# Kernel tuning notes

Measured on AMD Instinct MI355X. Metric: run time of the kernel, lower is better.

Reference implementation:

```python
import jax, jax.numpy as jnp
import numpy as np

DIM = 6
S = 2 ** DIM  # 64 nonzero B-spline basis products per edge (degree-1 spline)


def _bits():
    # [S, DIM] binary offsets enumerating the 2^dim corners of the spline cell
    return jnp.asarray(((np.arange(S)[:, None] >> np.arange(DIM)[None, :]) & 1).astype(np.int32))


def spline_basis(u, ks):
    # u: [E, DIM] pseudo-coords in [0,1); open B-spline, degree 1
    bits = _bits()                      # [S, DIM]
    v = u * (ks - 1)                    # [E, DIM]
    lo = jnp.floor(v)
    frac = v - lo                       # fractional position in cell
    lo = lo.astype(jnp.int32)
    # basis[e,s] = prod_d (frac if bit else 1-frac)
    basis = jnp.prod(jnp.where(bits[None].astype(bool), frac[:, None, :], 1.0 - frac[:, None, :]), axis=-1)  # [E,S]
    pos = jnp.clip(lo[:, None, :] + bits[None, :, :], 0, ks - 1)  # [E,S,DIM]
    strides = (ks ** jnp.arange(DIM)).astype(jnp.int32)           # per-dim stride in flattened kernel
    idx = jnp.sum(pos * strides[None, None, :], axis=-1)          # [E,S] in [0, ks^DIM)
    return basis, idx


def spline_conv(x, src, dst, basis, idx, W, Wr, b, n):
    # x:[N,in], W:[K,in,out], basis/idx:[E,S]. Mean aggregation + root weight + bias (PyG defaults).
    x_src = x[src]                                  # [E,in] gather
    out_ch = W.shape[2]
    acc0 = jnp.zeros((x_src.shape[0], out_ch), x.dtype)

    def body(acc, bs_is):
        bs, ii = bs_is                              # [E], [E]
        m = jnp.einsum('ei,eio->eo', x_src, W[ii])  # basis-indexed weight gather + per-edge matvec
        return acc + bs[:, None] * m, None

    msg, _ = jax.lax.scan(body, acc0, (basis.T, idx.T))   # loop over S=64 spline corners
    agg = jax.ops.segment_sum(msg, dst, num_segments=n)   # scatter-add to target nodes
    deg = jax.ops.segment_sum(jnp.ones(dst.shape, x.dtype), dst, num_segments=n)
    agg = agg / jnp.clip(deg, 1.0)[:, None]                # aggr='mean'
    return agg + x @ Wr + b


def setup_inputs() -> dict:
    key = jax.random.key(0)
    ks = jax.random.split(key, 16)
    N, E = 4096, 16384
    x = jax.random.normal(ks[0], (N, 32), jnp.float32)
    edge_index = jax.random.randint(ks[1], (2, E), 0, N, jnp.int32)
    edge_attr = jax.random.uniform(ks[2], (E, DIM), jnp.float32)

    def wk(k, K, cin, cout):
        return jax.random.normal(k, (K, cin, cout), jnp.float32) * (1.0 / np.sqrt(cin * S))

    def wr(k, cin, cout):
        return jax.random.normal(k, (cin, cout), jnp.float32) * (1.0 / np.sqrt(cin))

    return {
        'x': x, 'edge_index': edge_index, 'edge_attr': edge_attr,
        'W1': wk(ks[3], 3 ** DIM, 32, 128), 'Wr1': wr(ks[4], 32, 128), 'b1': jnp.zeros((128,), jnp.float32),
        'W3': wk(ks[5], 3 ** DIM, 128, 128), 'Wr3': wr(ks[6], 128, 128), 'b3': jnp.zeros((128,), jnp.float32),
        'W6': wk(ks[7], 5 ** DIM, 128, 64), 'Wr6': wr(ks[8], 128, 64), 'b6': jnp.zeros((64,), jnp.float32),
        'W7': wk(ks[9], 7 ** DIM, 64, 13), 'Wr7': wr(ks[10], 64, 13), 'b7': jnp.zeros((13,), jnp.float32),
    }


def reference(x, edge_index, edge_attr, W1, Wr1, b1, W3, Wr3, b3, W6, Wr6, b6, W7, Wr7, b7):
    src, dst = edge_index[0], edge_index[1]
    n = x.shape[0]
    basis3, idx3 = spline_basis(edge_attr, 3)  # shared by conv1 and conv3 (same kernel_size)
    h = spline_conv(x, src, dst, basis3, idx3, W1, Wr1, b1, n)
    h = spline_conv(h, src, dst, basis3, idx3, W3, Wr3, b3, n)
    basis5, idx5 = spline_basis(edge_attr, 5)
    h = spline_conv(h, src, dst, basis5, idx5, W6, Wr6, b6, n)
    basis7, idx7 = spline_basis(edge_attr, 7)
    h = spline_conv(h, src, dst, basis7, idx7, W7, Wr7, b7, n)
    h = jax.nn.elu(h)
    return jax.nn.log_softmax(h, axis=1)
```

## Files before the change

kernel.cpp:

```cpp
#include <hip/hip_runtime.h>
#include <hip/hip_bf16.h>
#include <cstdint>
#include <cstddef>

constexpr int SDIM = 6;
constexpr int SCOR = 64;
constexpr int REP3 = 8;
constexpr int CAP3 = 4096;
constexpr int CAP5 = 512;
constexpr int CAP7 = 128;
typedef unsigned short u16;
typedef unsigned char u8;
typedef __attribute__((ext_vector_type(8))) short bf16x8;
typedef __attribute__((ext_vector_type(4))) float f32x4;
typedef __attribute__((ext_vector_type(2))) float f32x2;
typedef __attribute__((ext_vector_type(4))) int i32x4;

__device__ __forceinline__ float bf2f(u16 h) {
    union { unsigned u; float f; } v; v.u = ((unsigned)h) << 16; return v.f;
}
__device__ __forceinline__ u16 f2bf(float f) {
    union { float f; unsigned u; } v; v.f = f;
    unsigned r = v.u + 0x7fffu + ((v.u >> 16) & 1u);
    return (u16)(r >> 16);
}

__device__ __forceinline__ u8 f2e4m3(float f) {
#if __has_builtin(__builtin_amdgcn_cvt_pk_fp8_f32)
    return (u8)(__builtin_amdgcn_cvt_pk_fp8_f32(f, 0.0f, 0, false) & 0xff);
#else
    unsigned u = __float_as_uint(f);
    unsigned s = (u >> 24) & 0x80;
    int exp = (int)((u >> 23) & 0xff) - 127;
    unsigned man = u & 0x7fffff;
    if (exp > 8 || (exp == 8 && man >= 0x700000)) return (u8)(s | 0x7e);
    if (exp >= -6) {
        unsigned m = man >> 20;
        unsigned rest = man & 0xfffff;
        if (rest > 0x80000 || (rest == 0x80000 && (m & 1))) m++;
        unsigned v = (((unsigned)(exp + 7)) << 3) + m;
        if (v > 0x7e) v = 0x7e;
        return (u8)(s | v);
    }
    if (exp < -10) return (u8)s;
    float af = __uint_as_float(u & 0x7fffffff);
    int M = (int)(af * 512.0f + 0.5f);
    if (M > 7) M = 7;
    return (u8)(s | M);
#endif
}

__device__ __forceinline__ void e4m3x4_acc(unsigned w, float* a) {
#if __has_builtin(__builtin_amdgcn_cvt_pk_f32_fp8)
    f32x2 lo = __builtin_amdgcn_cvt_pk_f32_fp8((int)w, false);
    f32x2 hi = __builtin_amdgcn_cvt_pk_f32_fp8((int)w, true);
    a[0] += lo.x; a[1] += lo.y; a[2] += hi.x; a[3] += hi.y;
#else
    #pragma unroll
    for (int j = 0; j < 4; j++) {
        unsigned b = (w >> (8 * j)) & 0xff;
        unsigned s = (b & 0x80) << 24;
        unsigned em = b & 0x7f;
        float v = (em >= 8)
            ? __uint_as_float((((em >> 3) + 120) << 23) | ((em & 7) << 20))
            : (float)em * (1.0f / 512.0f);
        a[j] += __uint_as_float(__float_as_uint(v) | s);
    }
#endif
}

template <int KS>
__device__ __forceinline__ void keybasis(const float* u, int s, int& key, float& basis) {
    int idx = 0, str = 1;
    float b = 1.0f;
    #pragma unroll
    for (int d = 0; d < SDIM; d++) {
        float v = u[d] * (KS - 1);
        float fl = floorf(v);
        float fr = v - fl;
        int bit = (s >> d) & 1;
        int pos = (int)fl + bit;
        pos = min(max(pos, 0), KS - 1);
        idx += pos * str;
        str *= KS;
        b *= bit ? fr : (1.0f - fr);
    }
    key = idx;
    basis = b;
}

__global__ __launch_bounds__(256) void prep_kernel(int* __restrict__ zb, int nz,
                                                   const float* __restrict__ xin,
                                                   u16* __restrict__ xbf, int n4) {
    int i = blockIdx.x * blockDim.x + threadIdx.x;
    if (i < nz) zb[i] = 0;
    if (i < n4) {
        float4 v = ((const float4*)xin)[i];
        ushort4 o;
        o.x = f2bf(v.x); o.y = f2bf(v.y); o.z = f2bf(v.z); o.w = f2bf(v.w);
        ((ushort4*)xbf)[i] = o;
    }
}

__global__ __launch_bounds__(256) void deg_kernel(const int* __restrict__ dst,
                                                  int* __restrict__ degi, int E) {
    int e = blockIdx.x * blockDim.x + threadIdx.x;
    if (e < E) atomicAdd(&degi[dst[e]], 1);
}

__global__ __launch_bounds__(1024) void scan_kernel(int* __restrict__ counts,
                                                    int* __restrict__ offs, int K) {
    __shared__ int sums[1024];
    int t = threadIdx.x;
    int chunk = (K + 1023) / 1024;
    int a0 = t * chunk;
    int a1 = min(a0 + chunk, K);
    int s = 0;
    for (int j = a0; j < a1; j++) s += counts[j];
    sums[t] = s;
    __syncthreads();
    for (int off = 1; off < 1024; off <<= 1) {
        int v = (t >= off) ? sums[t - off] : 0;
        __syncthreads();
        sums[t] += v;
        __syncthreads();
    }
    int run = (t == 0) ? 0 : sums[t - 1];
    for (int j = a0; j < a1; j++) {
        int c = counts[j];
        offs[j] = run;
        counts[j] = run;
        run += c;
    }
    if (t == 1023) offs[K] = run;
}

__global__ __launch_bounds__(256) void fill_all(const float* __restrict__ ea,
                                                const int* __restrict__ src,
                                                const int* __restrict__ dst,
                                                int* __restrict__ ecur,
                                                int* __restrict__ cnt3r, int2* __restrict__ pP3,
                                                int* __restrict__ cnt5, int2* __restrict__ pP5,
                                                int* __restrict__ cnt7, int2* __restrict__ pP7,
                                                int P) {
    int gid = blockIdx.x * blockDim.x + threadIdx.x;
    if (gid >= P) return;
    int e = gid >> 6;
    int lane = threadIdx.x & 63;
    int rep = blockIdx.x & (REP3 - 1);
    float u[SDIM];
    #pragma unroll
    for (int d = 0; d < SDIM; d++) u[d] = ea[e * SDIM + d];
    int node = src[e];
    int er = 0;
    if (lane == 0) er = atomicAdd(&ecur[dst[e]], 1);
    er = __shfl(er, 0);
    int packed = (node << 20) | (er * SCOR + lane);
    int k; float b; int slot;
    keybasis<3>(u, lane, k, b);
    slot = (k * REP3 + rep) * CAP3 + atomicAdd(&cnt3r[k * REP3 + rep], 1);
    pP3[slot] = make_int2(packed, __float_as_int(b));
    keybasis<5>(u, lane, k, b);
    slot = k * CAP5 + atomicAdd(&cnt5[k], 1);
    pP5[slot] = make_int2(packed, __float_as_int(b));
    keybasis<7>(u, lane, k, b);
    slot = k * CAP7 + atomicAdd(&cnt7[k], 1);
    pP7[slot] = make_int2(packed, __float_as_int(b));
}

template <int IN, int OUT, int WAVES, int WN, int CAP>
__global__ __launch_bounds__(WAVES * 64) void conv_mfma_r(
    const u16* __restrict__ xbf, const float* __restrict__ W,
    const int* __restrict__ cnt, const int2* __restrict__ pairP,
    u8* __restrict__ mpart) {
    constexpr int NT = WAVES * 64;
    constexpr int WM = WAVES / WN;
    constexpr int OUT16 = (OUT + 15) & ~15;
    static_assert(OUT == OUT16, "conv_mfma_r requires OUT multiple of 16");
    constexpr int WSTR = OUT + 2;
    constexpr int NF = OUT16 / 16;
    constexpr int NFW = NF / WN;
    constexpr int KS = IN / 32;
    constexpr int TW = NFW * 16;
    constexpr int TSTR = TW + 16;
    constexpr int CHW = TW / 16;
    static_assert(TSTR % 16 == 0, "row stride must be 16B aligned");
    static_assert((IN * OUT) % NT == 0, "staging divisibility");

    __shared__ u16 Wlds[IN * WSTR];
    __shared__ u8 tall[WAVES][16 * TSTR];

    int k = blockIdx.x;
    int idx = k * gridDim.y + blockIdx.y;
    int p0 = idx * CAP;
    int p1 = p0 + cnt[idx];
    if (p0 >= p1) return;

    int t = threadIdx.x;
    int wid = t >> 6, lane = t & 63;
    int wm = wid % WM, wn = wid / WM;
    int l15 = lane & 15, l4 = lane >> 4;
    u8* twave = tall[wid];

    const float* Wg = W + (size_t)k * IN * OUT;
    #pragma unroll
    for (int f0 = 0; f0 < IN * OUT; f0 += NT) {
        int f = f0 + t;
        int i = f / OUT, o = f % OUT;
        Wlds[i * WSTR + o] = f2bf(Wg[f]);
    }
    __syncthreads();

    bf16x8 breg[KS][NFW];
    #pragma unroll
    for (int ks = 0; ks < KS; ks++) {
        #pragma unroll
        for (int nf = 0; nf < NFW; nf++) {
            int col = (wn * NFW + nf) * 16 + l15;
            int rbase = ks * 32 + l4 * 8;
            bf16x8 b;
            #pragma unroll
            for (int j = 0; j < 8; j++)
                ((u16*)&b)[j] = Wlds[(rbase + j) * WSTR + col];
            breg[ks][nf] = b;
        }
    }

    constexpr int STRIDE = WM * 16;
    int t0 = p0 + wm * 16;
    if (t0 >= p1) return;

    int2 meta = pairP[min(t0 + l15, p1 - 1)];
    bf16x8 a[KS];
    {
        const u16* xrow = xbf + (size_t)((unsigned)meta.x >> 20) * IN + l4 * 8;
        #pragma unroll
        for (int ks = 0; ks < KS; ks++) a[ks] = *(const bf16x8*)(xrow + ks * 32);
    }

    while (true) {
        int np = min(16, p1 - t0);
        float basv = (l15 < np) ? __int_as_float(meta.y) * 64.0f : 0.0f;
        int srv = meta.x & 0xFFFFF;
        int tn = t0 + STRIDE;
        bool has = tn < p1;
        int2 metaN = meta;
        if (has) metaN = pairP[min(tn + l15, p1 - 1)];

        f32x4 acc[NFW];
        #pragma unroll
        for (int nf = 0; nf < NFW; nf++)
            acc[nf] = f32x4{0.f, 0.f, 0.f, 0.f};
        #pragma unroll
        for (int ks = 0; ks < KS; ks++) {
            #pragma unroll
            for (int nf = 0; nf < NFW; nf++)
                acc[nf] = __builtin_amdgcn_mfma_f32_16x16x32_bf16(a[ks], breg[ks][nf], acc[nf], 0, 0, 0);
        }

        bf16x8 aN[KS];
        if (has) {
            const u16* xrowN = xbf + (size_t)((unsigned)metaN.x >> 20) * IN + l4 * 8;
            #pragma unroll
            for (int ks = 0; ks < KS; ks++) aN[ks] = *(const bf16x8*)(xrowN + ks * 32);
        }

        #pragma unroll
        for (int nf = 0; nf < NFW; nf++) {
            #pragma unroll
            for (int r = 0; r < 4; r++) {
                int pl = l4 * 4 + r;
                float bs = __shfl(basv, pl);
                twave[pl * TSTR + nf * 16 + l15] = f2e4m3(acc[nf][r] * bs);
            }
        }

        #pragma unroll
        for (int it = 0; it < (16 * CHW + 63) / 64; it++) {
            int cid = it * 64 + lane;
            int row = cid / CHW, ch = cid % CHW;
            int srr = __shfl(srv, row);
            if (cid < 16 * CHW && row < np)
                __builtin_nontemporal_store(
                    *(const i32x4*)&twave[row * TSTR + ch * 16],
                    (i32x4*)(mpart + (size_t)srr * OUT16 + wn * TW + ch * 16));
        }

        if (!has) break;
        t0 = tn;
        meta = metaN;
        #pragma unroll
        for (int ks = 0; ks < KS; ks++) a[ks] = aN[ks];
    }
}

__global__ __launch_bounds__(256) void conv_mfma_w7(
    const u16* __restrict__ xbf, const float* __restrict__ W,
    const int* __restrict__ cnt, const int2* __restrict__ pairP,
    u16* __restrict__ mpart, int K) {
    constexpr int IN = 64, OUT = 13, OUT16 = 16;
    __shared__ u16 WT[4][16 * 72];
    __shared__ u16 tbAll[4][16 * 24];
    int t = threadIdx.x, wid = t >> 6, lane = t & 63;
    int k = blockIdx.x * 4 + wid;
    if (k >= K) return;
    int p0 = k * CAP7, p1 = p0 + cnt[k];
    if (p0 >= p1) return;
    u16* tb = tbAll[wid];
    u16* wt = WT[wid];

    int l15 = lane & 15, l4 = lane >> 4;
    const float* Wg = W + (size_t)k * (IN * OUT);
    for (int f = lane; f < IN * OUT; f += 64) {
        int r = f / OUT, c = f - r * OUT;
        wt[c * 72 + r] = f2bf(Wg[f]);
    }
    bf16x8 breg[2];
    #pragma unroll
    for (int ks = 0; ks < 2; ks++)
        breg[ks] = (l15 < OUT) ? *(const bf16x8*)&wt[l15 * 72 + ks * 32 + l4 * 8]
                               : bf16x8{0, 0, 0, 0, 0, 0, 0, 0};

    for (int t0 = p0; t0 < p1; t0 += 16) {
        int np = min(16, p1 - t0);
        int2 meta = pairP[min(t0 + l15, p1 - 1)];
        float basv = (l15 < np) ? __int_as_float(meta.y) : 0.0f;
        int srv = meta.x & 0xFFFFF;
        const u16* xrow = xbf + (size_t)((unsigned)meta.x >> 20) * IN + l4 * 8;
        f32x4 acc = f32x4{0.f, 0.f, 0.f, 0.f};
        #pragma unroll
        for (int ks = 0; ks < 2; ks++) {
            bf16x8 a = *(const bf16x8*)(xrow + ks * 32);
            acc = __builtin_amdgcn_mfma_f32_16x16x32_bf16(a, breg[ks], acc, 0, 0, 0);
        }
        #pragma unroll
        for (int r = 0; r < 4; r++) {
            int pl = l4 * 4 + r;
            float bs = __shfl(basv, pl);
            tb[pl * 24 + l15] = f2bf(acc[r] * bs);
        }
        {
            int row = lane >> 1, ch = lane & 1;
            int srr = __shfl(srv, row);
            if (lane < np * 2)
                __builtin_nontemporal_store(
                    *(const bf16x8*)&tb[row * 24 + ch * 8],
                    (bf16x8*)(mpart + (size_t)srr * OUT16 + ch * 8));
        }
    }
}

template <int IN, int OUT, int OUT16, bool HEAD, bool FP8>
__global__ __launch_bounds__(256) void reduce_wave(
    const void* __restrict__ mpartv, const int* __restrict__ eoff,
    const float* __restrict__ xin, const float* __restrict__ Wr,
    const float* __restrict__ bias, float* __restrict__ hout,
    u16* __restrict__ hbf, int N) {
    constexpr int CH = OUT16 / 16;
    constexpr int RG = 64 / CH;
    __shared__ float sm[4][OUT16];

    int t = threadIdx.x, wid = t >> 6, lane = t & 63;
    int nodeLocal = wid >> 1, hf = wid & 1;
    int n = blockIdx.x * 2 + nodeLocal;

    int e0 = 0, e1 = 0;
    if (n < N) { e0 = eoff[n]; e1 = eoff[n + 1]; }
    int R = (e1 - e0) * SCOR;
    size_t rs = (size_t)e0 * SCOR;
    int rg = lane / CH, ch = lane % CH;

    float a[16];
    #pragma unroll
    for (int j = 0; j < 16; j++) a[j] = 0.0f;
    #pragma unroll 4
    for (int r = rg + hf * RG; r < R; r += RG * 2) {
        if constexpr (FP8) {
            const u8* mp = (const u8*)mpartv + (rs + r) * OUT16 + ch * 16;
            i32x4 w = __builtin_nontemporal_load((const i32x4*)mp);
            e4m3x4_acc((unsigned)w.x, a + 0);
            e4m3x4_acc((unsigned)w.y, a + 4);
            e4m3x4_acc((unsigned)w.z, a + 8);
            e4m3x4_acc((unsigned)w.w, a + 12);
        } else {
            const u16* mp = (const u16*)mpartv + (rs + r) * OUT16 + ch * 16;
            bf16x8 v0 = __builtin_nontemporal_load((const bf16x8*)mp);
            bf16x8 v1 = __builtin_nontemporal_load((const bf16x8*)(mp + 8));
            #pragma unroll
            for (int j = 0; j < 8; j++) a[j] += bf2f(((const u16*)&v0)[j]);
            #pragma unroll
            for (int j = 0; j < 8; j++) a[8 + j] += bf2f(((const u16*)&v1)[j]);
        }
    }
    #pragma unroll
    for (int m = CH; m < 64; m <<= 1) {
        #pragma unroll
        for (int j = 0; j < 16; j++) a[j] += __shfl_xor(a[j], m);
    }
    if (lane < CH) {
        #pragma unroll
        for (int j = 0; j < 16; j++) sm[wid][lane * 16 + j] = a[j];
    }
    __syncthreads();

    if (n >= N) return;
    int dg = e1 - e0;
    float dinv = 1.0f / (float)(dg < 1 ? 1 : dg);
    if constexpr (FP8) dinv *= (1.0f / 64.0f);
    const float* xr = xin + (size_t)n * IN;

    if constexpr (!HEAD) {
        int o = hf * (OUT / 2) + lane;
        if (lane < OUT / 2) {
            float s = (sm[nodeLocal * 2][o] + sm[nodeLocal * 2 + 1][o]) * dinv + bias[o];
            #pragma unroll 8
            for (int i = 0; i < IN; i++) s += xr[i] * Wr[i * OUT + o];
            hout[(size_t)n * OUT + o] = s;
            if (hbf) hbf[(size_t)n * OUT + o] = f2bf(s);
        }
    } else {
        if (hf == 0 && lane < 16) {
            float s = 0.0f;
            if (lane < OUT) {
                s = (sm[nodeLocal * 2][lane] + sm[nodeLocal * 2 + 1][lane]) * dinv + bias[lane];
                #pragma unroll 8
                for (int i = 0; i < IN; i++) s += xr[i] * Wr[i * OUT + lane];
            }
            sm[wid][lane] = s;
            float v[13];
            float mx = -1e30f;
            #pragma unroll
            for (int c = 0; c < 13; c++) {
                float z = sm[wid][c];
                z = z > 0.0f ? z : (expf(z) - 1.0f);
                v[c] = z;
                mx = fmaxf(mx, z);
            }
            float sum = 0.0f;
            #pragma unroll
            for (int c = 0; c < 13; c++) sum += expf(v[c] - mx);
            float lse = mx + logf(sum);
            if (lane < 13) hout[(size_t)n * 13 + lane] = v[lane] - lse;
        }
    }
}

extern "C" void kernel_launch(void* const* d_in, const int* in_sizes, int n_in,
                              void* d_out, int out_size, void* d_ws, size_t ws_size,
                              hipStream_t stream) {
    const float* x   = (const float*)d_in[0];
    const int*   ei  = (const int*)d_in[1];
    const float* ea  = (const float*)d_in[2];
    const float* W1  = (const float*)d_in[3];
    const float* Wr1 = (const float*)d_in[4];
    const float* b1  = (const float*)d_in[5];
    const float* W3  = (const float*)d_in[6];
    const float* Wr3 = (const float*)d_in[7];
    const float* b3  = (const float*)d_in[8];
    const float* W6  = (const float*)d_in[9];
    const float* Wr6 = (const float*)d_in[10];
    const float* b6  = (const float*)d_in[11];
    const float* W7  = (const float*)d_in[12];
    const float* Wr7 = (const float*)d_in[13];
    const float* b7  = (const float*)d_in[14];

    const int N = in_sizes[0] / 32;
    const int E = in_sizes[1] / 2;
    const int* src = ei;
    const int* dst = ei + E;
    (void)n_in; (void)out_size; (void)ws_size;

    const int K3 = 729, K5 = 15625, K7 = 117649;
    const int P = E * SCOR;

    const int NC3 = K3 * REP3;
    const int totalZ = N + NC3 + K5 + K7;

    char* ws = (char*)d_ws;
    size_t off = 0;
    auto alloc = [&](size_t bytes) {
        void* p = ws + off;
        off += (bytes + 255) & ~(size_t)255;
        return p;
    };
    int*   zb    = (int*)alloc((size_t)totalZ * 4);
    int*   degi  = zb;
    int*   cnt3r = zb + N;
    int*   cnt5  = cnt3r + NC3;
    int*   cnt7  = cnt5 + K5;
    int*   eoff  = (int*)alloc((size_t)(N + 1) * 4);
    int2*  pP3   = (int2*)alloc((size_t)NC3 * CAP3 * 8);
    int2*  pP5   = (int2*)alloc((size_t)K5 * CAP5 * 8);
    int2*  pP7   = (int2*)alloc((size_t)K7 * CAP7 * 8);
    float* h1    = (float*)alloc((size_t)N * 128 * 4);
    float* h3    = (float*)alloc((size_t)N * 128 * 4);
    float* h6    = (float*)alloc((size_t)N * 64 * 4);
    u16*   xbf1  = (u16*)alloc((size_t)N * 32 * 2);
    u16*   hbf1  = (u16*)alloc((size_t)N * 128 * 2);
    u16*   hbf3  = (u16*)alloc((size_t)N * 128 * 2);
    u16*   hbf6  = (u16*)alloc((size_t)N * 64 * 2);
    u8*    mpart = (u8*)alloc((size_t)P * 128);

    dim3 blk(256);
    dim3 egrid((E + 255) / 256);
    dim3 pgrid((P + 255) / 256);
    int rgrid = (N + 1) / 2;

    int n4 = N * 32 / 4;
    prep_kernel<<<(max(totalZ, n4) + 255) / 256, blk, 0, stream>>>(zb, totalZ, x, xbf1, n4);

    deg_kernel<<<egrid, blk, 0, stream>>>(dst, degi, E);
    scan_kernel<<<1, 1024, 0, stream>>>(degi, eoff, N);

    fill_all<<<pgrid, blk, 0, stream>>>(ea, src, dst, degi, cnt3r, pP3, cnt5, pP5, cnt7, pP7, P);

    conv_mfma_r<32, 128, 8, 2, CAP3><<<dim3(K3, REP3), dim3(512), 0, stream>>>(
        xbf1, W1, cnt3r, pP3, mpart);
    reduce_wave<32, 128, 128, false, true><<<rgrid, blk, 0, stream>>>(mpart, eoff, x, Wr1, b1, h1, hbf1, N);

    conv_mfma_r<128, 128, 8, 2, CAP3><<<dim3(K3, REP3), dim3(512), 0, stream>>>(
        hbf1, W3, cnt3r, pP3, mpart);
    reduce_wave<128, 128, 128, false, true><<<rgrid, blk, 0, stream>>>(mpart, eoff, h1, Wr3, b3, h3, hbf3, N);

    conv_mfma_r<128, 64, 4, 2, CAP5><<<dim3(K5, 1), blk, 0, stream>>>(
        hbf3, W6, cnt5, pP5, mpart);
    reduce_wave<128, 64, 64, false, true><<<rgrid, blk, 0, stream>>>(mpart, eoff, h3, Wr6, b6, h6, hbf6, N);

    conv_mfma_w7<<<(K7 + 3) / 4, blk, 0, stream>>>(hbf6, W7, cnt7, pP7, (u16*)mpart, K7);
    reduce_wave<64, 13, 16, true, false><<<rgrid, blk, 0, stream>>>(mpart, eoff, h6, Wr7, b7, (float*)d_out, nullptr, N);
}
```

Measured before the change: 945.0 us.

## Replace CSR edge offsets with fixed-capacity per-node slots and bf16 root inputs

Drops the degree-count and single-block scan kernels. Each node now gets a fixed CAPN=32 slot region in the partial-message buffer, and the edge rank comes straight from the atomic in fill_all. The pair metadata is repacked so the basis is stored as bf16 next to a 16-bit source node, and the root-weight path reads bf16 activations instead of keeping separate fp32 copies. This removes two serial launches and some fp32 traffic, but it assumes in-degree ≤32 and node ids below 65536, enlarges mpart, and lowers basis and root-input precision.

Result: no change. 933.2 us (-1.3%).

```diff
diff --git a/kernel.cpp b/kernel.cpp
--- a/kernel.cpp
+++ b/kernel.cpp
@@ -9,6 +9,7 @@
 constexpr int CAP3 = 4096;
 constexpr int CAP5 = 512;
 constexpr int CAP7 = 128;
+constexpr int CAPN = 32;
 typedef unsigned short u16;
 typedef unsigned char u8;
 typedef __attribute__((ext_vector_type(8))) short bf16x8;
@@ -102,43 +103,10 @@
     }
 }
 
-__global__ __launch_bounds__(256) void deg_kernel(const int* __restrict__ dst,
-                                                  int* __restrict__ degi, int E) {
-    int e = blockIdx.x * blockDim.x + threadIdx.x;
-    if (e < E) atomicAdd(&degi[dst[e]], 1);
-}
-
-__global__ __launch_bounds__(1024) void scan_kernel(int* __restrict__ counts,
-                                                    int* __restrict__ offs, int K) {
-    __shared__ int sums[1024];
-    int t = threadIdx.x;
-    int chunk = (K + 1023) / 1024;
-    int a0 = t * chunk;
-    int a1 = min(a0 + chunk, K);
-    int s = 0;
-    for (int j = a0; j < a1; j++) s += counts[j];
-    sums[t] = s;
-    __syncthreads();
-    for (int off = 1; off < 1024; off <<= 1) {
-        int v = (t >= off) ? sums[t - off] : 0;
-        __syncthreads();
-        sums[t] += v;
-        __syncthreads();
-    }
-    int run = (t == 0) ? 0 : sums[t - 1];
-    for (int j = a0; j < a1; j++) {
-        int c = counts[j];
-        offs[j] = run;
-        counts[j] = run;
-        run += c;
-    }
-    if (t == 1023) offs[K] = run;
-}
-
 __global__ __launch_bounds__(256) void fill_all(const float* __restrict__ ea,
                                                 const int* __restrict__ src,
                                                 const int* __restrict__ dst,
-                                                int* __restrict__ ecur,
+                                                int* __restrict__ degi,
                                                 int* __restrict__ cnt3r, int2* __restrict__ pP3,
                                                 int* __restrict__ cnt5, int2* __restrict__ pP5,
                                                 int* __restrict__ cnt7, int2* __restrict__ pP7,
@@ -152,20 +120,26 @@
     #pragma unroll
     for (int d = 0; d < SDIM; d++) u[d] = ea[e * SDIM + d];
     int node = src[e];
+    int dn = dst[e];
     int er = 0;
-    if (lane == 0) er = atomicAdd(&ecur[dst[e]], 1);
+    if (lane == 0) er = atomicAdd(&degi[dn], 1);
     er = __shfl(er, 0);
-    int packed = (node << 20) | (er * SCOR + lane);
+    int er64 = (dn * CAPN + er) * SCOR + lane;
     int k; float b; int slot;
     keybasis<3>(u, lane, k, b);
+    int2 m;
+    m.x = er64;
+    m.y = ((int)f2bf(b) << 16) | node;
     slot = (k * REP3 + rep) * CAP3 + atomicAdd(&cnt3r[k * REP3 + rep], 1);
-    pP3[slot] = make_int2(packed, __float_as_int(b));
+    pP3[slot] = m;
     keybasis<5>(u, lane, k, b);
+    m.y = ((int)f2bf(b) << 16) | node;
     slot = k * CAP5 + atomicAdd(&cnt5[k], 1);
-    pP5[slot] = make_int2(packed, __float_as_int(b));
+    pP5[slot] = m;
     keybasis<7>(u, lane, k, b);
+    m.y = ((int)f2bf(b) << 16) | node;
     slot = k * CAP7 + atomicAdd(&cnt7[k], 1);
-    pP7[slot] = make_int2(packed, __float_as_int(b));
+    pP7[slot] = m;
 }
 
 template <int IN, int OUT, int WAVES, int WN, int CAP>
@@ -233,15 +207,15 @@
     int2 meta = pairP[min(t0 + l15, p1 - 1)];
     bf16x8 a[KS];
     {
-        const u16* xrow = xbf + (size_t)((unsigned)meta.x >> 20) * IN + l4 * 8;
+        const u16* xrow = xbf + (size_t)((unsigned)meta.y & 0xFFFF) * IN + l4 * 8;
         #pragma unroll
         for (int ks = 0; ks < KS; ks++) a[ks] = *(const bf16x8*)(xrow + ks * 32);
     }
 
     while (true) {
         int np = min(16, p1 - t0);
-        float basv = (l15 < np) ? __int_as_float(meta.y) * 64.0f : 0.0f;
-        int srv = meta.x & 0xFFFFF;
+        float basv = (l15 < np) ? bf2f((u16)((unsigned)meta.y >> 16)) * 64.0f : 0.0f;
+        int srv = meta.x;
         int tn = t0 + STRIDE;
         bool has = tn < p1;
         int2 metaN = meta;
@@ -260,7 +234,7 @@
 
         bf16x8 aN[KS];
         if (has) {
-            const u16* xrowN = xbf + (size_t)((unsigned)metaN.x >> 20) * IN + l4 * 8;
+            const u16* xrowN = xbf + (size_t)((unsigned)metaN.y & 0xFFFF) * IN + l4 * 8;
             #pragma unroll
             for (int ks = 0; ks < KS; ks++) aN[ks] = *(const bf16x8*)(xrowN + ks * 32);
         }
@@ -324,9 +298,9 @@
     for (int t0 = p0; t0 < p1; t0 += 16) {
         int np = min(16, p1 - t0);
         int2 meta = pairP[min(t0 + l15, p1 - 1)];
-        float basv = (l15 < np) ? __int_as_float(meta.y) : 0.0f;
-        int srv = meta.x & 0xFFFFF;
-        const u16* xrow = xbf + (size_t)((unsigned)meta.x >> 20) * IN + l4 * 8;
+        float basv = (l15 < np) ? bf2f((u16)((unsigned)meta.y >> 16)) : 0.0f;
+        int srv = meta.x;
+        const u16* xrow = xbf + (size_t)((unsigned)meta.y & 0xFFFF) * IN + l4 * 8;
         f32x4 acc = f32x4{0.f, 0.f, 0.f, 0.f};
         #pragma unroll
         for (int ks = 0; ks < 2; ks++) {
@@ -352,9 +326,9 @@
 
 template <int IN, int OUT, int OUT16, bool HEAD, bool FP8>
 __global__ __launch_bounds__(256) void reduce_wave(
-    const void* __restrict__ mpartv, const int* __restrict__ eoff,
-    const float* __restrict__ xin, const float* __restrict__ Wr,
-    const float* __restrict__ bias, float* __restrict__ hout,
+    const void* __restrict__ mpartv, const int* __restrict__ degi,
+    const u16* __restrict__ xinbf, const float* __restrict__ Wr,
+    const float* __restrict__ bias, float* __restrict__ outf,
     u16* __restrict__ hbf, int N) {
     constexpr int CH = OUT16 / 16;
     constexpr int RG = 64 / CH;
@@ -364,10 +338,9 @@
     int nodeLocal = wid >> 1, hf = wid & 1;
     int n = blockIdx.x * 2 + nodeLocal;
 
-    int e0 = 0, e1 = 0;
-    if (n < N) { e0 = eoff[n]; e1 = eoff[n + 1]; }
-    int R = (e1 - e0) * SCOR;
-    size_t rs = (size_t)e0 * SCOR;
+    int dg = (n < N) ? degi[n] : 0;
+    int R = dg * SCOR;
+    size_t rs = (size_t)n * CAPN * SCOR;
     int rg = lane / CH, ch = lane % CH;
 
     float a[16];
@@ -404,19 +377,17 @@
     __syncthreads();
 
     if (n >= N) return;
-    int dg = e1 - e0;
     float dinv = 1.0f / (float)(dg < 1 ? 1 : dg);
     if constexpr (FP8) dinv *= (1.0f / 64.0f);
-    const float* xr = xin + (size_t)n * IN;
+    const u16* xr = xinbf + (size_t)n * IN;
 
     if constexpr (!HEAD) {
         int o = hf * (OUT / 2) + lane;
         if (lane < OUT / 2) {
             float s = (sm[nodeLocal * 2][o] + sm[nodeLocal * 2 + 1][o]) * dinv + bias[o];
             #pragma unroll 8
-            for (int i = 0; i < IN; i++) s += xr[i] * Wr[i * OUT + o];
-            hout[(size_t)n * OUT + o] = s;
-            if (hbf) hbf[(size_t)n * OUT + o] = f2bf(s);
+            for (int i = 0; i < IN; i++) s += bf2f(xr[i]) * Wr[i * OUT + o];
+            hbf[(size_t)n * OUT + o] = f2bf(s);
         }
     } else {
         if (hf == 0 && lane < 16) {
@@ -424,7 +395,7 @@
             if (lane < OUT) {
                 s = (sm[nodeLocal * 2][lane] + sm[nodeLocal * 2 + 1][lane]) * dinv + bias[lane];
                 #pragma unroll 8
-                for (int i = 0; i < IN; i++) s += xr[i] * Wr[i * OUT + lane];
+                for (int i = 0; i < IN; i++) s += bf2f(xr[i]) * Wr[i * OUT + lane];
             }
             sm[wid][lane] = s;
             float v[13];
@@ -440,7 +411,7 @@
             #pragma unroll
             for (int c = 0; c < 13; c++) sum += expf(v[c] - mx);
             float lse = mx + logf(sum);
-            if (lane < 13) hout[(size_t)n * 13 + lane] = v[lane] - lse;
+            if (lane < 13) outf[(size_t)n * 13 + lane] = v[lane] - lse;
         }
     }
 }
@@ -488,44 +459,40 @@
     int*   cnt3r = zb + N;
     int*   cnt5  = cnt3r + NC3;
     int*   cnt7  = cnt5 + K5;
-    int*   eoff  = (int*)alloc((size_t)(N + 1) * 4);
     int2*  pP3   = (int2*)alloc((size_t)NC3 * CAP3 * 8);
     int2*  pP5   = (int2*)alloc((size_t)K5 * CAP5 * 8);
     int2*  pP7   = (int2*)alloc((size_t)K7 * CAP7 * 8);
-    float* h1    = (float*)alloc((size_t)N * 128 * 4);
-    float* h3    = (float*)alloc((size_t)N * 128 * 4);
-    float* h6    = (float*)alloc((size_t)N * 64 * 4);
     u16*   xbf1  = (u16*)alloc((size_t)N * 32 * 2);
     u16*   hbf1  = (u16*)alloc((size_t)N * 128 * 2);
     u16*   hbf3  = (u16*)alloc((size_t)N * 128 * 2);
     u16*   hbf6  = (u16*)alloc((size_t)N * 64 * 2);
-    u8*    mpart = (u8*)alloc((size_t)P * 128);
+    u8*    mpart = (u8*)alloc((size_t)N * CAPN * SCOR * 128);
 
     dim3 blk(256);
-    dim3 egrid((E + 255) / 256);
     dim3 pgrid((P + 255) / 256);
     int rgrid = (N + 1) / 2;
 
     int n4 = N * 32 / 4;
     prep_kernel<<<(max(totalZ, n4) + 255) / 256, blk, 0, stream>>>(zb, totalZ, x, xbf1, n4);
 
-    deg_kernel<<<egrid, blk, 0, stream>>>(dst, degi, E);
-    scan_kernel<<<1, 1024, 0, stream>>>(degi, eoff, N);
-
     fill_all<<<pgrid, blk, 0, stream>>>(ea, src, dst, degi, cnt3r, pP3, cnt5, pP5, cnt7, pP7, P);
 
     conv_mfma_r<32, 128, 8, 2, CAP3><<<dim3(K3, REP3), dim3(512), 0, stream>>>(
         xbf1, W1, cnt3r, pP3, mpart);
-    reduce_wave<32, 128, 128, false, true><<<rgrid, blk, 0, stream>>>(mpart, eoff, x, Wr1, b1, h1, hbf1, N);
+    reduce_wave<32, 128, 128, false, true><<<rgrid, blk, 0, stream>>>(
+        mpart, degi, xbf1, Wr1, b1, nullptr, hbf1, N);
 
     conv_mfma_r<128, 128, 8, 2, CAP3><<<dim3(K3, REP3), dim3(512), 0, stream>>>(
         hbf1, W3, cnt3r, pP3, mpart);
-    reduce_wave<128, 128, 128, false, true><<<rgrid, blk, 0, stream>>>(mpart, eoff, h1, Wr3, b3, h3, hbf3, N);
+    reduce_wave<128, 128, 128, false, true><<<rgrid, blk, 0, stream>>>(
+        mpart, degi, hbf1, Wr3, b3, nullptr, hbf3, N);
 
     conv_mfma_r<128, 64, 4, 2, CAP5><<<dim3(K5, 1), blk, 0, stream>>>(
         hbf3, W6, cnt5, pP5, mpart);
-    reduce_wave<128, 64, 64, false, true><<<rgrid, blk, 0, stream>>>(mpart, eoff, h3, Wr6, b6, h6, hbf6, N);
+    reduce_wave<128, 64, 64, false, true><<<rgrid, blk, 0, stream>>>(
+        mpart, degi, hbf3, Wr6, b6, nullptr, hbf6, N);
 
     conv_mfma_w7<<<(K7 + 3) / 4, blk, 0, stream>>>(hbf6, W7, cnt7, pP7, (u16*)mpart, K7);
-    reduce_wave<64, 13, 16, true, false><<<rgrid, blk, 0, stream>>>(mpart, eoff, h6, Wr7, b7, (float*)d_out, nullptr, N);
-}
+    reduce_wave<64, 13, 16, true, false><<<rgrid, blk, 0, stream>>>(
+        mpart, degi, hbf6, Wr7, b7, (float*)d_out, nullptr, N);
+}
```
